# Performance work log

Measured on AMD Instinct MI355X. Metric: run time of the kernel, lower is better.

The kernel has to match this reference:

```python
import jax, jax.numpy as jnp
import numpy as np

N_NODES = 100000
N_EDGES = 1600000
C_IN = 128
C_OUT = 64
BN_EPS = 1e-5
LEAKY_SLOPE = 0.01


def setup_inputs() -> dict:
    key = jax.random.key(0)
    k1, k2, k3 = jax.random.split(key, 3)
    x = jax.random.normal(k1, (N_NODES, C_IN), dtype=jnp.float32)
    edge_index = jax.random.randint(k2, (2, N_EDGES), 0, N_NODES, dtype=jnp.int32)
    W = jax.random.normal(k3, (C_IN, C_OUT), dtype=jnp.float32) * (1.0 / np.sqrt(C_IN))
    b = jnp.zeros((C_OUT,), dtype=jnp.float32)
    gamma = jnp.ones((C_OUT,), dtype=jnp.float32)
    beta = jnp.zeros((C_OUT,), dtype=jnp.float32)
    return {"x": x, "edge_index": edge_index, "W": W, "b": b, "gamma": gamma, "beta": beta}


def reference(x, edge_index, W, b, gamma, beta):
    n = x.shape[0]
    # --- GCNConv: add self-loops, symmetric normalization ---
    loop = jnp.arange(n, dtype=edge_index.dtype)
    row = jnp.concatenate([edge_index[0], loop])  # source
    col = jnp.concatenate([edge_index[1], loop])  # target
    deg = jax.ops.segment_sum(jnp.ones_like(col, dtype=x.dtype), col, num_segments=n)
    deg_inv_sqrt = jnp.where(deg > 0, jax.lax.rsqrt(deg), 0.0)
    norm = deg_inv_sqrt[row] * deg_inv_sqrt[col]  # [E+N]
    xw = x @ W  # [N, C_OUT] - transform before aggregation (PyG GCNConv)
    msgs = xw[row] * norm[:, None]  # [E+N, C_OUT]
    out = jax.ops.segment_sum(msgs, col, num_segments=n) + b  # [N, C_OUT]
    # --- BatchNorm (training mode: batch stats over nodes, biased var) ---
    mean = jnp.mean(out, axis=0)
    var = jnp.mean(jnp.square(out - mean), axis=0)
    y = gamma * (out - mean) * jax.lax.rsqrt(var + BN_EPS) + beta
    # --- LeakyReLU (default negative_slope=0.01); dropout p=0 is identity ---
    return jnp.where(y >= 0, y, LEAKY_SLOPE * y)
```

## Files before the change

### kernel.cpp

```cpp
#include <hip/hip_runtime.h>

#define C_IN 128
#define C_OUT 64
#define BN_EPS 1e-5f
#define LEAKY 0.01f

#define BSZ   256
#define NBMAX 512
#define CAP   6144
#define CHUNKA 2048
#define NPART 16

using bf16x8 = __attribute__((ext_vector_type(8))) __bf16;
using f32x4  = __attribute__((ext_vector_type(4))) float;

__device__ inline unsigned short f2b(float f) {
    unsigned u = __float_as_uint(f);
    return (unsigned short)((u + 0x7fffu + ((u >> 16) & 1u)) >> 16);
}
__device__ inline float b2f(unsigned short b) {
    return __uint_as_float(((unsigned)b) << 16);
}

__global__ __launch_bounds__(256) void k_prep(const float* __restrict__ W,
                                              unsigned short* __restrict__ wb,
                                              int* __restrict__ bfill,
                                              float* __restrict__ part) {
    int idx = blockIdx.x * 256 + threadIdx.x;
    if (idx < NBMAX) bfill[idx] = 0;
    if (idx < NPART * 128) part[idx] = 0.f;
    if (idx >= C_IN * C_OUT) return;
    int k = idx >> 6, col = idx & 63;
    int t = col >> 4, nlo = col & 15;
    int c = k >> 5, q = (k >> 3) & 3, j = k & 7;
    wb[(size_t)((((t * 4 + c) * 4 + q) * 16) + nlo) * 8 + j] = f2b(W[idx]);
}

__global__ __launch_bounds__(256) void k_binA(const int* __restrict__ rows,
                                              const int* __restrict__ cols,
                                              int* __restrict__ bfill,
                                              unsigned* __restrict__ pairs,
                                              int nE, int NB) {
    __shared__ int hist[NBMAX];
    __shared__ int base[NBMAX];
    __shared__ int lstart[NBMAX];
    __shared__ int cursor[NBMAX];
    __shared__ unsigned lpair[CHUNKA];
    __shared__ unsigned short lbkt[CHUNKA];
    __shared__ unsigned lsorted[CHUNKA];
    __shared__ unsigned short lsbkt[CHUNKA];
    int t = threadIdx.x;
    int chunk = blockIdx.x * CHUNKA;
    int cnt = min(chunk + CHUNKA, nE) - chunk;

    hist[t] = 0; hist[t + 256] = 0;
    __syncthreads();

    for (int i = t; i < cnt; i += 256) {
        int c = cols[chunk + i];
        unsigned r = (unsigned)rows[chunk + i];
        int b = c >> 8;
        lpair[i] = ((unsigned)(c & (BSZ - 1)) << 24) | r;
        lbkt[i] = (unsigned short)b;
        atomicAdd(&hist[b], 1);
    }
    __syncthreads();

    int h0 = hist[t], h1 = hist[t + 256];
    if (t < NB && h0) base[t] = atomicAdd(&bfill[t], h0);
    if (t + 256 < NB && h1) base[t + 256] = atomicAdd(&bfill[t + 256], h1);
    lstart[t] = h0; lstart[t + 256] = h1;
    __syncthreads();
    for (int off = 1; off < 512; off <<= 1) {
        int a = (t >= off) ? lstart[t - off] : 0;
        int bb = lstart[t + 256 - off];
        __syncthreads();
        lstart[t] += a; lstart[t + 256] += bb;
        __syncthreads();
    }
    int s0 = lstart[t] - h0, s1 = lstart[t + 256] - h1;
    lstart[t] = s0; lstart[t + 256] = s1;
    cursor[t] = s0; cursor[t + 256] = s1;
    __syncthreads();

    for (int i = t; i < cnt; i += 256) {
        int b = lbkt[i];
        int pos = atomicAdd(&cursor[b], 1);
        lsorted[pos] = lpair[i];
        lsbkt[pos] = (unsigned short)b;
    }
    __syncthreads();

    for (int i = t; i < cnt; i += 256) {
        int b = lsbkt[i];
        int off = base[b] + (i - lstart[b]);
        if (off < CAP)
            pairs[(size_t)b * CAP + off] = lsorted[i];
    }
}

__global__ __launch_bounds__(256) void k_binB(const int* __restrict__ bfill,
                                              const unsigned* __restrict__ pairs,
                                              int2* __restrict__ pd,
                                              int* __restrict__ srcs, int n) {
    __shared__ unsigned rowbuf[CAP];
    __shared__ int sorted[CAP];
    __shared__ int histL[BSZ];
    __shared__ int scanL[BSZ];
    int b = blockIdx.x;
    int t = threadIdx.x;
    int cnt = min(bfill[b], CAP);
    const unsigned* reg = pairs + (size_t)b * CAP;

    histL[t] = 0;
    __syncthreads();
    for (int i = t; i < cnt; i += 256) {
        unsigned p = reg[i];
        rowbuf[i] = p;
        atomicAdd(&histL[p >> 24], 1);
    }
    __syncthreads();

    int hv = histL[t];
    scanL[t] = hv;
    __syncthreads();
    for (int off = 1; off < 256; off <<= 1) {
        int x = (t >= off) ? scanL[t - off] : 0;
        __syncthreads();
        scanL[t] += x;
        __syncthreads();
    }
    int my_start = scanL[t] - hv;

    int s0 = b * CAP;
    int node = (b << 8) + t;
    if (node < n) pd[node] = make_int2(s0 + my_start, hv);
    __syncthreads();
    histL[t] = my_start;
    __syncthreads();
    for (int i = t; i < cnt; i += 256) {
        unsigned p = rowbuf[i];
        int pos = atomicAdd(&histL[p >> 24], 1);
        sorted[pos] = (int)(p & 0xFFFFFFu);
    }
    __syncthreads();
    for (int i = t; i < cnt; i += 256)
        srcs[s0 + i] = sorted[i];
}

__global__ __launch_bounds__(256) void k_gemm(const float* __restrict__ x,
                                              const unsigned short* __restrict__ wb,
                                              const int2* __restrict__ pd,
                                              unsigned short* __restrict__ xwsb, int n) {
    const int lane = threadIdx.x & 63;
    const int wave = threadIdx.x >> 6;
    const int base = (blockIdx.x * 4 + wave) * 16;
    if (base >= n) return;

    const int nlo  = lane & 15;
    const int quad = lane >> 4;

    const bf16x8* Wv = (const bf16x8*)wb;
    bf16x8 Bf[4][4];
    #pragma unroll
    for (int t = 0; t < 4; ++t)
        #pragma unroll
        for (int c = 0; c < 4; ++c)
            Bf[t][c] = Wv[((t * 4 + c) * 4 + quad) * 16 + nlo];

    f32x4 acc[4] = {};
    int m = base + nlo;
    const float* xrow = x + (size_t)(m < n ? m : n - 1) * C_IN;

    #pragma unroll
    for (int c = 0; c < 4; ++c) {
        float4 a0 = *(const float4*)&xrow[c * 32 + quad * 8];
        float4 a1 = *(const float4*)&xrow[c * 32 + quad * 8 + 4];
        bf16x8 Af;
        Af[0] = (__bf16)a0.x; Af[1] = (__bf16)a0.y;
        Af[2] = (__bf16)a0.z; Af[3] = (__bf16)a0.w;
        Af[4] = (__bf16)a1.x; Af[5] = (__bf16)a1.y;
        Af[6] = (__bf16)a1.z; Af[7] = (__bf16)a1.w;
        #pragma unroll
        for (int t = 0; t < 4; ++t)
            acc[t] = __builtin_amdgcn_mfma_f32_16x16x32_bf16(Af, Bf[t][c], acc[t], 0, 0, 0);
    }

    #pragma unroll
    for (int r = 0; r < 4; ++r) {
        int node = base + quad * 4 + r;
        if (node < n) {
            float dn = rsqrtf((float)(pd[node].y + 1));
            #pragma unroll
            for (int t = 0; t < 4; ++t)
                xwsb[(size_t)node * C_OUT + t * 16 + nlo] = f2b(acc[t][r] * dn);
        }
    }
}

#define ACC8(d) do { \
    acc[0] += __uint_as_float((d).x << 16); \
    acc[1] += __uint_as_float((d).x & 0xffff0000u); \
    acc[2] += __uint_as_float((d).y << 16); \
    acc[3] += __uint_as_float((d).y & 0xffff0000u); \
    acc[4] += __uint_as_float((d).z << 16); \
    acc[5] += __uint_as_float((d).z & 0xffff0000u); \
    acc[6] += __uint_as_float((d).w << 16); \
    acc[7] += __uint_as_float((d).w & 0xffff0000u); } while (0)

__global__ __launch_bounds__(256) void k_gather(const int2* __restrict__ pd,
                                                const int* __restrict__ srcs,
                                                const unsigned short* __restrict__ xwsb,
                                                float* __restrict__ out,
                                                float* __restrict__ part, int n) {
    __shared__ float sredS[16][64];
    __shared__ float sredQ[16][64];
    int lane = threadIdx.x & 63;
    int wv   = threadIdx.x >> 6;
    int s    = lane & 7;
    int g    = (lane >> 3) & 1;
    int q    = lane >> 4;
    int l16  = lane & 15;
    int c0 = s * 8 + ((lane & 8) ? 4 : 0);
    const uint4* xw16 = (const uint4*)xwsb;

    int node = blockIdx.x * 16 + wv * 4 + q;
    bool active = node < n;

    int2 p = active ? pd[node] : make_int2(0, 0);
    int dg = p.y;
    float dn = rsqrtf((float)(dg + 1));
    uint2 selfu = active ? *(const uint2*)&xwsb[(size_t)node * C_OUT + c0]
                         : make_uint2(0u, 0u);

    float acc[8] = {0.f, 0.f, 0.f, 0.f, 0.f, 0.f, 0.f, 0.f};

    int sv = (active && l16 < dg) ? srcs[p.x + l16] : 0;
    for (int b2 = 0;;) {
        int m = dg - b2;
        #pragma unroll
        for (int j = 0; j < 8; ++j) {
            int idx = j * 2 + g;
            int src = __shfl(sv, (lane & 48) + idx);
            if (idx < m) {
                uint4 d = xw16[((size_t)src << 3) + s];
                ACC8(d);
            }
        }
        b2 += 16;
        if (b2 >= dg) break;
        sv = (l16 < dg - b2) ? srcs[p.x + b2 + l16] : 0;
    }

    #pragma unroll
    for (int k = 0; k < 4; ++k) {
        float send = (lane & 8) ? acc[k] : acc[k + 4];
        float recv = __shfl_xor(send, 8);
        acc[k] = ((lane & 8) ? acc[k + 4] : acc[k]) + recv;
    }

    float v0 = active ? (acc[0] + __uint_as_float(selfu.x << 16)) * dn : 0.f;
    float v1 = active ? (acc[1] + __uint_as_float(selfu.x & 0xffff0000u)) * dn : 0.f;
    float v2 = active ? (acc[2] + __uint_as_float(selfu.y << 16)) * dn : 0.f;
    float v3 = active ? (acc[3] + __uint_as_float(selfu.y & 0xffff0000u)) * dn : 0.f;

    if (active)
        *(float4*)&out[(size_t)node * C_OUT + c0] = make_float4(v0, v1, v2, v3);

    int slot = wv * 4 + q;
    sredS[slot][c0 + 0] = v0;       sredQ[slot][c0 + 0] = v0 * v0;
    sredS[slot][c0 + 1] = v1;       sredQ[slot][c0 + 1] = v1 * v1;
    sredS[slot][c0 + 2] = v2;       sredQ[slot][c0 + 2] = v2 * v2;
    sredS[slot][c0 + 3] = v3;       sredQ[slot][c0 + 3] = v3 * v3;
    __syncthreads();
    int t = threadIdx.x;
    if (t < 128) {
        int cc = t & 63;
        float a = 0.f;
        if (t < 64) {
            #pragma unroll
            for (int j = 0; j < 16; ++j) a += sredS[j][cc];
        } else {
            #pragma unroll
            for (int j = 0; j < 16; ++j) a += sredQ[j][cc];
        }
        atomicAdd(&part[(blockIdx.x & (NPART - 1)) * 128 + t], a);
    }
}

__global__ __launch_bounds__(256) void k_final(const float* __restrict__ part,
                                               const float* __restrict__ gamma,
                                               const float* __restrict__ beta,
                                               float* __restrict__ out, int n) {
    __shared__ float lp[NPART * 128];
    __shared__ float tot[128];
    int t = threadIdx.x;
    #pragma unroll
    for (int r = 0; r < NPART * 128 / 256; ++r)
        lp[t + r * 256] = part[t + r * 256];
    __syncthreads();
    if (t < 128) {
        float a = 0.f;
        #pragma unroll
        for (int j = 0; j < NPART; ++j) a += lp[j * 128 + t];
        tot[t] = a;
    }
    __syncthreads();

    int gid = blockIdx.x * 256 + t;
    int total4 = n * (C_OUT / 4);
    if (gid >= total4) return;
    int c4 = (gid & 15) * 4;
    float inv_n = 1.0f / (float)n;
    float4 g4 = *(const float4*)&gamma[c4];
    float4 b4 = *(const float4*)&beta[c4];
    float4 v = ((const float4*)out)[gid];

    float m, var, k, y;
    m = tot[c4 + 0] * inv_n; var = tot[64 + c4 + 0] * inv_n - m * m;
    k = rsqrtf(var + BN_EPS) * g4.x;
    y = (v.x - m) * k + b4.x; v.x = y >= 0.f ? y : LEAKY * y;
    m = tot[c4 + 1] * inv_n; var = tot[64 + c4 + 1] * inv_n - m * m;
    k = rsqrtf(var + BN_EPS) * g4.y;
    y = (v.y - m) * k + b4.y; v.y = y >= 0.f ? y : LEAKY * y;
    m = tot[c4 + 2] * inv_n; var = tot[64 + c4 + 2] * inv_n - m * m;
    k = rsqrtf(var + BN_EPS) * g4.z;
    y = (v.z - m) * k + b4.z; v.z = y >= 0.f ? y : LEAKY * y;
    m = tot[c4 + 3] * inv_n; var = tot[64 + c4 + 3] * inv_n - m * m;
    k = rsqrtf(var + BN_EPS) * g4.w;
    y = (v.w - m) * k + b4.w; v.w = y >= 0.f ? y : LEAKY * y;

    ((float4*)out)[gid] = v;
}

extern "C" void kernel_launch(void* const* d_in, const int* in_sizes, int n_in,
                              void* d_out, int out_size, void* d_ws, size_t ws_size,
                              hipStream_t stream) {
    const float* x     = (const float*)d_in[0];
    const int*   ei    = (const int*)d_in[1];
    const float* W     = (const float*)d_in[2];
    const float* gamma = (const float*)d_in[4];
    const float* beta  = (const float*)d_in[5];
    float* out = (float*)d_out;

    int n  = in_sizes[0] / C_IN;
    int nE = in_sizes[1] / 2;
    const int* rows = ei;
    const int* cols = ei + nE;
    int NB = (n + BSZ - 1) / BSZ;

    int2* pd = (int2*)d_ws;
    unsigned short* xwsb = (unsigned short*)(pd + n);
    unsigned* pairs = (unsigned*)(xwsb + (size_t)n * C_OUT);
    int* srcs = (int*)pairs;
    int* bfill = (int*)(pairs + (size_t)NB * CAP);
    float* part = (float*)(bfill + NBMAX);
    unsigned short* wb = (unsigned short*)(part + NPART * 128);

    k_prep<<<(C_IN * C_OUT + 255) / 256, 256, 0, stream>>>(W, wb, bfill, part);
    k_binA<<<(nE + CHUNKA - 1) / CHUNKA, 256, 0, stream>>>(rows, cols, bfill, pairs, nE, NB);
    k_binB<<<NB, 256, 0, stream>>>(bfill, pairs, pd, srcs, n);
    k_gemm<<<(n + 63) / 64, 256, 0, stream>>>(x, wb, pd, xwsb, n);
    k_gather<<<(n + 15) / 16, 256, 0, stream>>>(pd, srcs, xwsb, out, part, n);
    k_final<<<(n * (C_OUT / 4) + 255) / 256, 256, 0, stream>>>(part, gamma, beta, out, n);
}
```

Before: 197.0 us.

## Map 8 lanes per node in gather kernel instead of 16

The gather kernel now assigns 8 lanes per destination node, each covering 8 channels through a 16-byte load. Previously 16 lanes per node split edges into two halves and merged them with a cross-lane shuffle. Each block now processes 32 nodes, so the per-block reduction buffers are padded to 65 columns to avoid shared-memory bank conflicts. This removes the shuffle reduction and doubles nodes per wave, at the cost of more serial edge iterations per lane and more register use.

```diff
diff --git a/kernel.cpp b/kernel.cpp
--- a/kernel.cpp
+++ b/kernel.cpp
@@ -213,65 +213,69 @@
                                                 const unsigned short* __restrict__ xwsb,
                                                 float* __restrict__ out,
                                                 float* __restrict__ part, int n) {
-    __shared__ float sredS[16][64];
-    __shared__ float sredQ[16][64];
+    __shared__ float sredS[32][65];
+    __shared__ float sredQ[32][65];
     int lane = threadIdx.x & 63;
     int wv   = threadIdx.x >> 6;
     int s    = lane & 7;
-    int g    = (lane >> 3) & 1;
-    int q    = lane >> 4;
-    int l16  = lane & 15;
-    int c0 = s * 8 + ((lane & 8) ? 4 : 0);
+    int o    = lane >> 3;
     const uint4* xw16 = (const uint4*)xwsb;
 
-    int node = blockIdx.x * 16 + wv * 4 + q;
+    int node = blockIdx.x * 32 + wv * 8 + o;
     bool active = node < n;
 
     int2 p = active ? pd[node] : make_int2(0, 0);
     int dg = p.y;
     float dn = rsqrtf((float)(dg + 1));
-    uint2 selfu = active ? *(const uint2*)&xwsb[(size_t)node * C_OUT + c0]
-                         : make_uint2(0u, 0u);
+    uint4 selfu = active ? xw16[(size_t)node * 8 + s] : make_uint4(0, 0, 0, 0);
 
     float acc[8] = {0.f, 0.f, 0.f, 0.f, 0.f, 0.f, 0.f, 0.f};
 
-    int sv = (active && l16 < dg) ? srcs[p.x + l16] : 0;
+    int sv0 = (active && s < dg) ? srcs[p.x + s] : 0;
+    int sv1 = (active && 8 + s < dg) ? srcs[p.x + 8 + s] : 0;
     for (int b2 = 0;;) {
         int m = dg - b2;
         #pragma unroll
         for (int j = 0; j < 8; ++j) {
-            int idx = j * 2 + g;
-            int src = __shfl(sv, (lane & 48) + idx);
-            if (idx < m) {
+            int src = __shfl(sv0, (o << 3) + j);
+            if (j < m) {
+                uint4 d = xw16[((size_t)src << 3) + s];
+                ACC8(d);
+            }
+        }
+        #pragma unroll
+        for (int j = 0; j < 8; ++j) {
+            int src = __shfl(sv1, (o << 3) + j);
+            if (8 + j < m) {
                 uint4 d = xw16[((size_t)src << 3) + s];
                 ACC8(d);
             }
         }
         b2 += 16;
         if (b2 >= dg) break;
-        sv = (l16 < dg - b2) ? srcs[p.x + b2 + l16] : 0;
-    }
-
+        sv0 = (s < dg - b2) ? srcs[p.x + b2 + s] : 0;
+        sv1 = (8 + s < dg - b2) ? srcs[p.x + b2 + 8 + s] : 0;
+    }
+
+    float v[8];
+    unsigned su[4] = {selfu.x, selfu.y, selfu.z, selfu.w};
     #pragma unroll
     for (int k = 0; k < 4; ++k) {
-        float send = (lane & 8) ? acc[k] : acc[k + 4];
-        float recv = __shfl_xor(send, 8);
-        acc[k] = ((lane & 8) ? acc[k + 4] : acc[k]) + recv;
-    }
-
-    float v0 = active ? (acc[0] + __uint_as_float(selfu.x << 16)) * dn : 0.f;
-    float v1 = active ? (acc[1] + __uint_as_float(selfu.x & 0xffff0000u)) * dn : 0.f;
-    float v2 = active ? (acc[2] + __uint_as_float(selfu.y << 16)) * dn : 0.f;
-    float v3 = active ? (acc[3] + __uint_as_float(selfu.y & 0xffff0000u)) * dn : 0.f;
-
-    if (active)
-        *(float4*)&out[(size_t)node * C_OUT + c0] = make_float4(v0, v1, v2, v3);
-
-    int slot = wv * 4 + q;
-    sredS[slot][c0 + 0] = v0;       sredQ[slot][c0 + 0] = v0 * v0;
-    sredS[slot][c0 + 1] = v1;       sredQ[slot][c0 + 1] = v1 * v1;
-    sredS[slot][c0 + 2] = v2;       sredQ[slot][c0 + 2] = v2 * v2;
-    sredS[slot][c0 + 3] = v3;       sredQ[slot][c0 + 3] = v3 * v3;
+        v[2 * k]     = (acc[2 * k]     + __uint_as_float(su[k] << 16)) * dn;
+        v[2 * k + 1] = (acc[2 * k + 1] + __uint_as_float(su[k] & 0xffff0000u)) * dn;
+    }
+    if (active) {
+        float4* op = (float4*)&out[(size_t)node * C_OUT + s * 8];
+        op[0] = make_float4(v[0], v[1], v[2], v[3]);
+        op[1] = make_float4(v[4], v[5], v[6], v[7]);
+    }
+
+    int slot = wv * 8 + o;
+    #pragma unroll
+    for (int k = 0; k < 8; ++k) {
+        sredS[slot][s * 8 + k] = v[k];
+        sredQ[slot][s * 8 + k] = v[k] * v[k];
+    }
     __syncthreads();
     int t = threadIdx.x;
     if (t < 128) {
@@ -279,10 +283,10 @@
         float a = 0.f;
         if (t < 64) {
             #pragma unroll
-            for (int j = 0; j < 16; ++j) a += sredS[j][cc];
+            for (int j = 0; j < 32; ++j) a += sredS[j][cc];
         } else {
             #pragma unroll
-            for (int j = 0; j < 16; ++j) a += sredQ[j][cc];
+            for (int j = 0; j < 32; ++j) a += sredQ[j][cc];
         }
         atomicAdd(&part[(blockIdx.x & (NPART - 1)) * 128 + t], a);
     }
@@ -361,6 +365,6 @@
     k_binA<<<(nE + CHUNKA - 1) / CHUNKA, 256, 0, stream>>>(rows, cols, bfill, pairs, nE, NB);
     k_binB<<<NB, 256, 0, stream>>>(bfill, pairs, pd, srcs, n);
     k_gemm<<<(n + 63) / 64, 256, 0, stream>>>(x, wb, pd, xwsb, n);
-    k_gather<<<(n + 15) / 16, 256, 0, stream>>>(pd, srcs, xwsb, out, part, n);
+    k_gather<<<(n + 31) / 32, 256, 0, stream>>>(pd, srcs, xwsb, out, part, n);
     k_final<<<(n * (C_OUT / 4) + 255) / 256, 256, 0, stream>>>(part, gamma, beta, out, n);
 }
```

Result: no change. 195.7 us (-0.7%).
